# Kernel optimization log

Hardware: AMD Instinct MI355X
Metric: run time of the kernel (lower is better)

The kernel has to match this reference:

```python
import jax, jax.numpy as jnp
import numpy as np

EMBED_DIM = 768
NUM_HEADS = 12
HEAD_DIM = EMBED_DIM // NUM_HEADS


def setup_inputs() -> dict:
    key = jax.random.key(0)
    ks = jax.random.split(key, 6)
    B, N = 8, 1024
    x = jax.random.normal(ks[0], (B, N, EMBED_DIM), dtype=jnp.float32)
    pos_embedding = jax.random.normal(ks[1], (1, NUM_HEADS, N, N), dtype=jnp.float32)
    s_in = 1.0 / np.sqrt(EMBED_DIM)
    W_qkv = jax.random.normal(ks[2], (EMBED_DIM, 3 * EMBED_DIM), dtype=jnp.float32) * s_in
    b_qkv = jnp.zeros((3 * EMBED_DIM,), dtype=jnp.float32)
    W_proj = jax.random.normal(ks[3], (EMBED_DIM, EMBED_DIM), dtype=jnp.float32) * s_in
    b_proj = jnp.zeros((EMBED_DIM,), dtype=jnp.float32)
    return {"x": x, "pos_embedding": pos_embedding, "W_qkv": W_qkv,
            "b_qkv": b_qkv, "W_proj": W_proj, "b_proj": b_proj}


def reference(x, pos_embedding, W_qkv, b_qkv, W_proj, b_proj):
    B, N, C = x.shape
    H, D = NUM_HEADS, HEAD_DIM
    qkv = x @ W_qkv + b_qkv                      # [B,N,3C]
    qkv = qkv.reshape(B, N, 3, H, D)
    q = qkv[:, :, 0].transpose(0, 2, 1, 3)       # [B,H,N,D]
    k = qkv[:, :, 1].transpose(0, 2, 1, 3)
    v = qkv[:, :, 2].transpose(0, 2, 1, 3)
    # NOTE: bias is added BEFORE scaling, matching the original module.
    scores = (jnp.einsum('bhnd,bhmd->bhnm', q, k) + pos_embedding) / jnp.sqrt(
        jnp.asarray(D, dtype=x.dtype))
    attn = jax.nn.softmax(scores, axis=-1)       # dropout is identity in eval
    out = jnp.einsum('bhnm,bhmd->bhnd', attn, v)
    out = out.transpose(0, 2, 1, 3).reshape(B, N, C)
    return out @ W_proj + b_proj
```

## Files before the change

kernel.cpp:

```cpp
#include <hip/hip_runtime.h>

#define SEQ   1024
#define HEADS 12
#define CDIM  768
#define BATCH 8

#define QSCALE 0.18033688011112042f

typedef __attribute__((ext_vector_type(8))) short bf16x8;
typedef __attribute__((ext_vector_type(4))) float f32x4;
typedef __attribute__((ext_vector_type(16))) float f32x16;
typedef __attribute__((ext_vector_type(4))) float float4v;
typedef __attribute__((ext_vector_type(4))) short short4v;

__device__ __forceinline__ void gload_lds16(const void* g, void* l) {
  __builtin_amdgcn_global_load_lds(
      (const __attribute__((address_space(1))) unsigned int*)g,
      (__attribute__((address_space(3))) unsigned int*)l, 16, 0, 0);
}

__device__ __forceinline__ unsigned short f2bf(float f) {
  union { float f; unsigned u; } v; v.f = f;
  unsigned r = v.u + 0x7fff + ((v.u >> 16) & 1);
  return (unsigned short)(r >> 16);
}

__device__ __forceinline__ unsigned cvtpk(float a, float b) {
  unsigned r;
  asm("v_cvt_pk_bf16_f32 %0, %1, %2" : "=v"(r) : "v"(a), "v"(b));
  return r;
}

__device__ __forceinline__ float bfsel(unsigned u, int odd) {
  union { unsigned u; float f; } v;
  v.u = odd ? (u & 0xffff0000u) : (u << 16);
  return v.f;
}

__global__ __launch_bounds__(256) void prep_x_kernel(const float* __restrict__ x,
                                                     short* __restrict__ A) {
  int i = blockIdx.x * 256 + threadIdx.x;
  int r = i / 192;
  int c4 = (i % 192) * 4;
  float4v xv = *(const float4v*)(x + (size_t)r * 768 + c4);
  short4v hi;
#pragma unroll
  for (int j = 0; j < 4; ++j) hi[j] = (short)f2bf(xv[j]);
  *(short4v*)(A + (size_t)r * 768 + c4) = hi;
}

__global__ __launch_bounds__(256) void prep_w_kernel(const float* __restrict__ W,
                                                     short* __restrict__ Bt) {
  __shared__ float tile[64][65];
  int k0 = blockIdx.x * 64;
  int n0 = blockIdx.y * 64;
  int t = threadIdx.x;
#pragma unroll
  for (int it = 0; it < 16; ++it) {
    int r = it * 4 + (t >> 6);
    int c = t & 63;
    tile[r][c] = W[(size_t)(k0 + r) * 2304 + n0 + c];
  }
  __syncthreads();
#pragma unroll
  for (int it = 0; it < 16; ++it) {
    int nr = it * 4 + (t >> 6);
    int kc = t & 63;
    Bt[(size_t)(n0 + nr) * 768 + k0 + kc] = (short)f2bf(tile[kc][nr]);
  }
}

__global__ __launch_bounds__(256) void prep_wp_kernel(const float* __restrict__ W,
                                                      short* __restrict__ Bt) {
  __shared__ float tile[64][65];
  int k0 = blockIdx.x * 64;
  int n0 = blockIdx.y * 64;
  int t = threadIdx.x;
#pragma unroll
  for (int it = 0; it < 16; ++it) {
    int r = it * 4 + (t >> 6);
    int c = t & 63;
    tile[r][c] = W[(size_t)(k0 + r) * 768 + n0 + c];
  }
  __syncthreads();
#pragma unroll
  for (int it = 0; it < 16; ++it) {
    int nr = it * 4 + (t >> 6);
    int kc = t & 63;
    Bt[(size_t)(n0 + nr) * 768 + k0 + kc] = (short)f2bf(tile[kc][nr]);
  }
}

__global__ __launch_bounds__(256) void prep_pos_kernel(const float* __restrict__ P,
                                                       short* __restrict__ PB) {
  int t = blockIdx.x * 256 + threadIdx.x;
  int lane = t & 63;
  int jh   = (t >> 6) & 1;
  int i0   = (t >> 7) & 1;
  int w    = (t >> 8) & 3;
  int ti   = (t >> 10) & 15;
  int qblk = (t >> 14) & 7;
  int h    = t >> 17;
  int c5 = lane & 31, g1 = lane >> 5;
  int q = qblk * 128 + w * 32 + c5;
  const float* src = P + ((size_t)h * SEQ + q) * SEQ
                     + ti * 64 + i0 * 32 + 4 * g1 + 16 * jh;
  float4v v0 = *(const float4v*)(src);
  float4v v1 = *(const float4v*)(src + 8);
  union { short s[8]; bf16x8 v; } o;
#pragma unroll
  for (int p = 0; p < 4; ++p) {
    o.s[p]     = (short)f2bf(v0[p] * QSCALE);
    o.s[4 + p] = (short)f2bf(v1[p] * QSCALE);
  }
  *(bf16x8*)(PB + (size_t)t * 8) = o.v;
}

template <int MODE>
__global__ __launch_bounds__(512, 6) void gemm_kernel(
    const short* __restrict__ A, const short* __restrict__ Bt,
    const float* __restrict__ bias,
    short* __restrict__ outQ, short* __restrict__ outK, short* __restrict__ outVT,
    float* __restrict__ outF) {
  constexpr int NBLK = (MODE == 1) ? 18 : 6;
  constexpr int CHUNK = (MODE == 1) ? 144 : 48;
  const int bid = blockIdx.x;
  const int lb = (bid & 7) * CHUNK + (bid >> 3);
  const int n0 = (lb % NBLK) * 128;
  const int m0 = (lb / NBLK) * 128;

  __shared__ short lds[3 * 8192];

  const int tid = threadIdx.x;
  const int lane = tid & 63;
  const int w = tid >> 6;
  const int wr = (w & 1) * 64;
  const int wc = (w >> 1) * 32;
  const int c = lane & 15, g = lane >> 4;
  f32x4 acc[4][2];
#pragma unroll
  for (int mi = 0; mi < 4; ++mi)
#pragma unroll
    for (int ni = 0; ni < 2; ++ni) acc[mi][ni] = (f32x4){0.f, 0.f, 0.f, 0.f};

  auto STAGE = [&](int buf, int k0) {
    short* base = lds + buf * 8192;
    int row = tid >> 2;
    int us = (tid & 3) ^ (row & 3);
    gload_lds16(A + (size_t)(m0 + row) * 768 + k0 + us * 8, base + w * 512);
    gload_lds16(Bt + (size_t)(n0 + row) * 768 + k0 + us * 8, base + 4096 + w * 512);
  };

  STAGE(0, 0);
  STAGE(1, 32);
  asm volatile("s_waitcnt vmcnt(2)" ::: "memory");
  __builtin_amdgcn_sched_barrier(0);
  __builtin_amdgcn_s_barrier();

  for (int t = 0; t < 24; ++t) {
    if (t < 22) STAGE((t + 2) % 3, (t + 2) * 32);
    const char* Ab = (const char*)(lds + (t % 3) * 8192);
    const char* Bb = Ab + 8192;
    __builtin_amdgcn_s_setprio(1);
    bf16x8 af[4], bfv[2];
#pragma unroll
    for (int mi = 0; mi < 4; ++mi) {
      int row = wr + mi * 16 + c;
      af[mi] = *(const bf16x8*)(Ab + row * 64 + ((g ^ (row & 3)) * 16));
    }
#pragma unroll
    for (int ni = 0; ni < 2; ++ni) {
      int row = wc + ni * 16 + c;
      bfv[ni] = *(const bf16x8*)(Bb + row * 64 + ((g ^ (row & 3)) * 16));
    }
#pragma unroll
    for (int mi = 0; mi < 4; ++mi)
#pragma unroll
      for (int ni = 0; ni < 2; ++ni)
        acc[mi][ni] = __builtin_amdgcn_mfma_f32_16x16x32_bf16(
            af[mi], bfv[ni], acc[mi][ni], 0, 0, 0);
    __builtin_amdgcn_s_setprio(0);
    if (t < 23) {
      if (t < 22) asm volatile("s_waitcnt vmcnt(2)" ::: "memory");
      else        asm volatile("s_waitcnt vmcnt(0)" ::: "memory");
      __builtin_amdgcn_sched_barrier(0);
      __builtin_amdgcn_s_barrier();
    }
  }

  if (MODE == 1) {
    const int three = n0 / 768;
    const int nb = n0 - three * 768;
#pragma unroll
    for (int mi = 0; mi < 4; ++mi)
#pragma unroll
      for (int ni = 0; ni < 2; ++ni)
#pragma unroll
        for (int j = 0; j < 4; ++j) {
          int row = m0 + wr + mi * 16 + (g << 2) + j;
          int col = n0 + wc + ni * 16 + c;
          float v = acc[mi][ni][j] + bias[col];
          int rem = nb + wc + ni * 16 + c;
          int hh = rem >> 6, d = rem & 63;
          int b = row >> 10, n = row & 1023;
          size_t bh = (size_t)(b * 12 + hh);
          if (three == 0)      outQ[(bh * 1024 + n) * 64 + d] = (short)f2bf(v * QSCALE);
          else if (three == 1) outK[(bh * 1024 + n) * 64 + d] = (short)f2bf(v);
          else                 outVT[(bh * 64 + d) * 1024 + n] = (short)f2bf(v);
        }
  } else {
#pragma unroll
    for (int mi = 0; mi < 4; ++mi)
#pragma unroll
      for (int ni = 0; ni < 2; ++ni)
#pragma unroll
        for (int j = 0; j < 4; ++j) {
          int row = m0 + wr + mi * 16 + (g << 2) + j;
          int col = n0 + wc + ni * 16 + c;
          outF[(size_t)row * 768 + col] = acc[mi][ni][j] + bias[col];
        }
  }
}

#define MKFRAG(B, pA, pB, pC, pD)                                    \
  { unsigned x0 = (pA), y0 = (pC), x1 = (pB), y1 = (pD);             \
    asm("v_permlane32_swap_b32 %0, %1" : "+v"(x0), "+v"(y0));        \
    asm("v_permlane32_swap_b32 %0, %1" : "+v"(x1), "+v"(y1));        \
    B.u[0] = x0; B.u[1] = x1; B.u[2] = y0; B.u[3] = y1; }

__global__ __launch_bounds__(256, 3) void attn_kernel(
    const short* __restrict__ qb, const short* __restrict__ kb,
    const short* __restrict__ vtb, const short* __restrict__ posb,
    short* __restrict__ outb) {
  const int bid = blockIdx.x;
  const int lb = (bid & 7) * 96 + (bid >> 3);
  const int qblk = lb & 7;
  const int hb = lb >> 3;
  const int h = hb >> 3, b = hb & 7;

  const int tid = threadIdx.x, lane = tid & 63, w = tid >> 6;
  const int c5 = lane & 31, g1 = lane >> 5;
  const size_t bh = (size_t)(b * 12 + h);
  const short* Q = qb + bh * SEQ * 64;
  const short* K = kb + bh * SEQ * 64;
  const short* VT = vtb + bh * 64 * SEQ;
  const int q0w = qblk * 128 + w * 32;

  const short* pwb = posb + (size_t)h * 1048576 + (size_t)qblk * 131072
                     + w * 2048 + lane * 8;

  __shared__ short kls[3 * 4096];
  __shared__ short vls[3 * 4096];

  bf16x8 qf[4];
#pragma unroll
  for (int kd = 0; kd < 4; ++kd)
    qf[kd] = *(const bf16x8*)(Q + (size_t)(q0w + c5) * 64 + kd * 16 + g1 * 8);

  f32x16 o0, o1;
#pragma unroll
  for (int i = 0; i < 16; ++i) { o0[i] = 0.f; o1[i] = 0.f; }
  float lsum = 0.f;

  auto STAGE = [&](short* kb_, short* vb_, int kv0) {
    int r0 = w * 8 + (lane >> 3);
    int u0 = (lane & 7) ^ (r0 & 7);
    gload_lds16(K + (size_t)(kv0 + r0) * 64 + u0 * 8, kb_ + w * 512);
    gload_lds16(K + (size_t)(kv0 + 32 + r0) * 64 + u0 * 8, kb_ + 2048 + w * 512);
    gload_lds16(VT + (size_t)r0 * SEQ + kv0 + u0 * 8, vb_ + w * 512);
    gload_lds16(VT + (size_t)(32 + r0) * SEQ + kv0 + u0 * 8, vb_ + 2048 + w * 512);
  };

  short* kbuf0 = kls;        short* vbuf0 = vls;
  short* kbuf1 = kls + 4096; short* vbuf1 = vls + 4096;
  short* kbuf2 = kls + 8192; short* vbuf2 = vls + 8192;

  STAGE(kbuf0, vbuf0, 0);
  STAGE(kbuf1, vbuf1, 64);
  asm volatile("s_waitcnt vmcnt(4)" ::: "memory");
  __builtin_amdgcn_sched_barrier(0);
  __builtin_amdgcn_s_barrier();

  for (int ti = 0; ti < 16; ++ti) {
    const int kv0 = ti * 64;

    union { bf16x8 v; unsigned u[4]; } ua0, ua1, ub0, ub1;
    ua0.v = *(const bf16x8*)(pwb + ti * 8192);
    ua1.v = *(const bf16x8*)(pwb + ti * 8192 + 512);
    ub0.v = *(const bf16x8*)(pwb + ti * 8192 + 1024);
    ub1.v = *(const bf16x8*)(pwb + ti * 8192 + 1536);
    asm volatile("" ::: "memory");
    if (ti < 14) STAGE(kbuf2, vbuf2, kv0 + 128);

    const short* kc = kbuf0;
    const short* vc = vbuf0;

    f32x16 p0, p1;
#pragma unroll
    for (int i = 0; i < 16; ++i) { p0[i] = 0.f; p1[i] = 0.f; }
    __builtin_amdgcn_s_setprio(1);
#pragma unroll
    for (int kd = 0; kd < 4; ++kd) {
      int off0 = (c5 * 128 + kd * 32 + g1 * 16) ^ ((c5 & 7) << 4);
      int off1 = ((32 + c5) * 128 + kd * 32 + g1 * 16) ^ ((c5 & 7) << 4);
      bf16x8 kf0 = *(const bf16x8*)((const char*)kc + off0);
      bf16x8 kf1 = *(const bf16x8*)((const char*)kc + off1);
      p0 = __builtin_amdgcn_mfma_f32_32x32x16_bf16(kf0, qf[kd], p0, 0, 0, 0);
      p1 = __builtin_amdgcn_mfma_f32_32x32x16_bf16(kf1, qf[kd], p1, 0, 0, 0);
    }
    __builtin_amdgcn_s_setprio(0);

#pragma unroll
    for (int r = 0; r < 16; ++r) {
      unsigned wa = (r < 8) ? ua0.u[(r >> 1) & 3] : ua1.u[(r >> 1) & 3];
      unsigned wb = (r < 8) ? ub0.u[(r >> 1) & 3] : ub1.u[(r >> 1) & 3];
      float a = exp2f(p0[r] + bfsel(wa, r & 1));
      float bq = exp2f(p1[r] + bfsel(wb, r & 1));
      p0[r] = a; p1[r] = bq;
      lsum += a + bq;
    }

    unsigned pk0[8], pk1[8];
#pragma unroll
    for (int m = 0; m < 4; ++m) {
      pk0[2 * m]     = cvtpk(p0[4 * m],     p0[4 * m + 1]);
      pk0[2 * m + 1] = cvtpk(p0[4 * m + 2], p0[4 * m + 3]);
      pk1[2 * m]     = cvtpk(p1[4 * m],     p1[4 * m + 1]);
      pk1[2 * m + 1] = cvtpk(p1[4 * m + 2], p1[4 * m + 3]);
    }

    union bb { bf16x8 v; unsigned u[4]; } B0, B1, B2, B3;
    MKFRAG(B0, pk0[0], pk0[1], pk0[2], pk0[3]);
    MKFRAG(B1, pk0[4], pk0[5], pk0[6], pk0[7]);
    MKFRAG(B2, pk1[0], pk1[1], pk1[2], pk1[3]);
    MKFRAG(B3, pk1[4], pk1[5], pk1[6], pk1[7]);

    __builtin_amdgcn_s_setprio(1);
#define PVSTEP(Bv, s)                                                        \
    { int o0f = (c5 * 128 + (s) * 32 + g1 * 16) ^ ((c5 & 7) << 4);           \
      int o1f = ((32 + c5) * 128 + (s) * 32 + g1 * 16) ^ ((c5 & 7) << 4);    \
      bf16x8 vf0 = *(const bf16x8*)((const char*)vc + o0f);                  \
      bf16x8 vf1 = *(const bf16x8*)((const char*)vc + o1f);                  \
      o0 = __builtin_amdgcn_mfma_f32_32x32x16_bf16(vf0, Bv.v, o0, 0, 0, 0);  \
      o1 = __builtin_amdgcn_mfma_f32_32x32x16_bf16(vf1, Bv.v, o1, 0, 0, 0); }
    PVSTEP(B0, 0); PVSTEP(B1, 1); PVSTEP(B2, 2); PVSTEP(B3, 3);
#undef PVSTEP
    __builtin_amdgcn_s_setprio(0);

    short* tk = kbuf0; kbuf0 = kbuf1; kbuf1 = kbuf2; kbuf2 = tk;
    short* tv = vbuf0; vbuf0 = vbuf1; vbuf1 = vbuf2; vbuf2 = tv;

    if (ti < 15) {
      if (ti < 14) asm volatile("s_waitcnt vmcnt(4)" ::: "memory");
      else         asm volatile("s_waitcnt vmcnt(0)" ::: "memory");
      __builtin_amdgcn_sched_barrier(0);
      __builtin_amdgcn_s_barrier();
    }
  }

  lsum += __shfl_xor(lsum, 32);
  float inv = 1.0f / lsum;
  size_t obase = (size_t)(b * SEQ + q0w + c5) * 768 + h * 64 + g1 * 4;
#pragma unroll
  for (int m = 0; m < 4; ++m) {
    short4v ov0, ov1;
#pragma unroll
    for (int j = 0; j < 4; ++j) {
      ov0[j] = (short)f2bf(o0[4 * m + j] * inv);
      ov1[j] = (short)f2bf(o1[4 * m + j] * inv);
    }
    *(short4v*)(outb + obase + m * 8) = ov0;
    *(short4v*)(outb + obase + 32 + m * 8) = ov1;
  }
}

extern "C" void kernel_launch(void* const* d_in, const int* in_sizes, int n_in,
                              void* d_out, int out_size, void* d_ws, size_t ws_size,
                              hipStream_t stream) {
  const float* x      = (const float*)d_in[0];
  const float* pos    = (const float*)d_in[1];
  const float* W_qkv  = (const float*)d_in[2];
  const float* b_qkv  = (const float*)d_in[3];
  const float* W_proj = (const float*)d_in[4];
  const float* b_proj = (const float*)d_in[5];
  float* out = (float*)d_out;

  char* ws = (char*)d_ws;
  short* A       = (short*)(ws);
  short* attnbuf = (short*)(ws);
  short* Bt      = (short*)(ws + 12582912);
  short* wpt     = (short*)(ws + 16121856);
  short* qbuf    = (short*)(ws + 17301504);
  short* kbuf    = (short*)(ws + 29884416);
  short* vtbuf   = (short*)(ws + 42467328);
  short* posb    = (short*)(ws + 55050240);

  prep_x_kernel<<<6144, 256, 0, stream>>>(x, A);
  prep_w_kernel<<<dim3(12, 36), 256, 0, stream>>>(W_qkv, Bt);
  prep_wp_kernel<<<dim3(12, 12), 256, 0, stream>>>(W_proj, wpt);
  prep_pos_kernel<<<6144, 256, 0, stream>>>(pos, posb);
  gemm_kernel<1><<<1152, 512, 0, stream>>>(A, Bt, b_qkv,
                                           qbuf, kbuf, vtbuf, nullptr);
  attn_kernel<<<768, 256, 0, stream>>>(qbuf, kbuf, vtbuf, posb, attnbuf);
  gemm_kernel<2><<<384, 512, 0, stream>>>(attnbuf, wpt, b_proj,
                                          nullptr, nullptr, nullptr, out);
}
```

Baseline: 153.6 us.

## Use 256x256 tiles with double-buffered LDS for the QKV projection GEMM

Splits the templated GEMM into a dedicated QKV kernel that computes 256x256 output tiles per 512-thread block, with a larger LDS double buffer (128KB) and swizzled fragment loads. Loads for the next k-tile are interleaved across four sub-phases of MFMA work. The aim is more operand reuse per global byte and fewer blocks. The cost is lower occupancy (2 blocks/CU bound, 288 blocks on a large-CU GPU, so a possible tail or underfill) and higher register pressure from 32 accumulators per lane.

```diff
diff --git a/kernel.cpp b/kernel.cpp
--- a/kernel.cpp
+++ b/kernel.cpp
@@ -116,14 +116,132 @@
   *(bf16x8*)(PB + (size_t)t * 8) = o.v;
 }
 
-template <int MODE>
-__global__ __launch_bounds__(512, 6) void gemm_kernel(
+__global__ __launch_bounds__(512, 2) void gemm1_kernel(
     const short* __restrict__ A, const short* __restrict__ Bt,
     const float* __restrict__ bias,
-    short* __restrict__ outQ, short* __restrict__ outK, short* __restrict__ outVT,
-    float* __restrict__ outF) {
-  constexpr int NBLK = (MODE == 1) ? 18 : 6;
-  constexpr int CHUNK = (MODE == 1) ? 144 : 48;
+    short* __restrict__ outQ, short* __restrict__ outK, short* __restrict__ outVT) {
+  const int bid = blockIdx.x;
+  const int lb = (bid & 7) * 36 + (bid >> 3);
+  const int nt = lb % 9, mt = lb / 9;
+  const int n0 = nt * 256, m0 = mt * 256;
+
+  __shared__ short lds[65536];
+
+  const int tid = threadIdx.x;
+  const int lane = tid & 63;
+  const int w = tid >> 6;
+  const int wm = w >> 2;
+  const int wn = w & 3;
+  const int c = lane & 15, g = lane >> 4;
+
+  f32x4 acc[8][4];
+#pragma unroll
+  for (int i = 0; i < 8; ++i)
+#pragma unroll
+    for (int v = 0; v < 4; ++v) acc[i][v] = (f32x4){0.f, 0.f, 0.f, 0.f};
+
+  const int rl = lane >> 3;
+  const int su = (lane & 7) ^ rl;
+
+  auto STAGE_A = [&](int db, int h, int kt) {
+    short* dst = lds + db * 32768 + h * 8192;
+    const short* src = A + (size_t)(m0 + h * 128) * 768 + kt * 64 + su * 8;
+    gload_lds16(src + (size_t)((w * 2 + 0) * 8 + rl) * 768, dst + (w * 2 + 0) * 512);
+    gload_lds16(src + (size_t)((w * 2 + 1) * 8 + rl) * 768, dst + (w * 2 + 1) * 512);
+  };
+  auto STAGE_B = [&](int db, int h, int kt) {
+    short* dst = lds + db * 32768 + 16384 + h * 8192;
+    const short* src = Bt + (size_t)(n0 + h * 128) * 768 + kt * 64 + su * 8;
+    gload_lds16(src + (size_t)((w * 2 + 0) * 8 + rl) * 768, dst + (w * 2 + 0) * 512);
+    gload_lds16(src + (size_t)((w * 2 + 1) * 8 + rl) * 768, dst + (w * 2 + 1) * 512);
+  };
+
+  STAGE_A(0, 0, 0); STAGE_A(0, 1, 0); STAGE_B(0, 0, 0); STAGE_B(0, 1, 0);
+  asm volatile("s_waitcnt vmcnt(2)" ::: "memory");
+  __builtin_amdgcn_sched_barrier(0);
+  __builtin_amdgcn_s_barrier();
+
+  for (int kt = 0; kt < 12; ++kt) {
+    const int d = kt & 1;
+    const char* Ab = (const char*)(lds + d * 32768 + wm * 8192);
+    const char* Bb = (const char*)(lds + d * 32768 + 16384);
+    bf16x8 af[4][2];
+#pragma unroll
+    for (int p = 0; p < 4; ++p) {
+      const int al = p >> 1, be = p & 1;
+      if (kt < 11) {
+        if (p == 0)      STAGE_A(d ^ 1, 0, kt + 1);
+        else if (p == 1) STAGE_A(d ^ 1, 1, kt + 1);
+        else if (p == 2) STAGE_B(d ^ 1, 0, kt + 1);
+        else             STAGE_B(d ^ 1, 1, kt + 1);
+      }
+      if (be == 0) {
+#pragma unroll
+        for (int i = 0; i < 4; ++i) {
+          int rloc = (al * 4 + i) * 16 + c;
+          int sw = (rloc & 7) << 4;
+#pragma unroll
+          for (int kk = 0; kk < 2; ++kk)
+            af[i][kk] = *(const bf16x8*)(Ab + ((rloc * 128 + kk * 64 + g * 16) ^ sw));
+        }
+      }
+      bf16x8 bfv[2][2];
+#pragma unroll
+      for (int v = 0; v < 2; ++v) {
+        int rloc = v * 64 + wn * 16 + c;
+        int sw = (rloc & 7) << 4;
+#pragma unroll
+        for (int kk = 0; kk < 2; ++kk)
+          bfv[v][kk] = *(const bf16x8*)(Bb + be * 16384 +
+                                        ((rloc * 128 + kk * 64 + g * 16) ^ sw));
+      }
+      __builtin_amdgcn_s_setprio(1);
+#pragma unroll
+      for (int i = 0; i < 4; ++i)
+#pragma unroll
+        for (int v = 0; v < 2; ++v)
+#pragma unroll
+          for (int kk = 0; kk < 2; ++kk)
+            acc[al * 4 + i][be * 2 + v] = __builtin_amdgcn_mfma_f32_16x16x32_bf16(
+                af[i][kk], bfv[v][kk], acc[al * 4 + i][be * 2 + v], 0, 0, 0);
+      __builtin_amdgcn_s_setprio(0);
+      if (p == 0) {
+        if (kt < 11) asm volatile("s_waitcnt vmcnt(2)" ::: "memory");
+        else         asm volatile("s_waitcnt vmcnt(0)" ::: "memory");
+      } else if (p == 3 && kt < 11) {
+        asm volatile("s_waitcnt vmcnt(2)" ::: "memory");
+      }
+      __builtin_amdgcn_sched_barrier(0);
+      __builtin_amdgcn_s_barrier();
+    }
+  }
+
+  const int three = (n0 >= 1536) ? 2 : ((n0 >= 768) ? 1 : 0);
+  const int nb = n0 - three * 768;
+#pragma unroll
+  for (int mi = 0; mi < 8; ++mi)
+#pragma unroll
+    for (int nu = 0; nu < 4; ++nu)
+#pragma unroll
+      for (int j = 0; j < 4; ++j) {
+        int row = m0 + wm * 128 + mi * 16 + (g << 2) + j;
+        int col = n0 + nu * 64 + wn * 16 + c;
+        float v = acc[mi][nu][j] + bias[col];
+        int rem = nb + nu * 64 + wn * 16 + c;
+        int hh = rem >> 6, dd = rem & 63;
+        int b = row >> 10, n = row & 1023;
+        size_t bh = (size_t)(b * 12 + hh);
+        if (three == 0)      outQ[(bh * 1024 + n) * 64 + dd] = (short)f2bf(v * QSCALE);
+        else if (three == 1) outK[(bh * 1024 + n) * 64 + dd] = (short)f2bf(v);
+        else                 outVT[(bh * 64 + dd) * 1024 + n] = (short)f2bf(v);
+      }
+}
+
+__global__ __launch_bounds__(512, 6) void gemm2_kernel(
+    const short* __restrict__ A, const short* __restrict__ Bt,
+    const float* __restrict__ bias, float* __restrict__ outF) {
+  constexpr int NBLK = 6;
+  constexpr int CHUNK = 48;
   const int bid = blockIdx.x;
   const int lb = (bid & 7) * CHUNK + (bid >> 3);
   const int n0 = (lb % NBLK) * 128;
@@ -188,38 +306,16 @@
     }
   }
 
-  if (MODE == 1) {
-    const int three = n0 / 768;
-    const int nb = n0 - three * 768;
-#pragma unroll
-    for (int mi = 0; mi < 4; ++mi)
-#pragma unroll
-      for (int ni = 0; ni < 2; ++ni)
-#pragma unroll
-        for (int j = 0; j < 4; ++j) {
-          int row = m0 + wr + mi * 16 + (g << 2) + j;
-          int col = n0 + wc + ni * 16 + c;
-          float v = acc[mi][ni][j] + bias[col];
-          int rem = nb + wc + ni * 16 + c;
-          int hh = rem >> 6, d = rem & 63;
-          int b = row >> 10, n = row & 1023;
-          size_t bh = (size_t)(b * 12 + hh);
-          if (three == 0)      outQ[(bh * 1024 + n) * 64 + d] = (short)f2bf(v * QSCALE);
-          else if (three == 1) outK[(bh * 1024 + n) * 64 + d] = (short)f2bf(v);
-          else                 outVT[(bh * 64 + d) * 1024 + n] = (short)f2bf(v);
-        }
-  } else {
-#pragma unroll
-    for (int mi = 0; mi < 4; ++mi)
-#pragma unroll
-      for (int ni = 0; ni < 2; ++ni)
-#pragma unroll
-        for (int j = 0; j < 4; ++j) {
-          int row = m0 + wr + mi * 16 + (g << 2) + j;
-          int col = n0 + wc + ni * 16 + c;
-          outF[(size_t)row * 768 + col] = acc[mi][ni][j] + bias[col];
-        }
-  }
+#pragma unroll
+  for (int mi = 0; mi < 4; ++mi)
+#pragma unroll
+    for (int ni = 0; ni < 2; ++ni)
+#pragma unroll
+      for (int j = 0; j < 4; ++j) {
+        int row = m0 + wr + mi * 16 + (g << 2) + j;
+        int col = n0 + wc + ni * 16 + c;
+        outF[(size_t)row * 768 + col] = acc[mi][ni][j] + bias[col];
+      }
 }
 
 #define MKFRAG(B, pA, pB, pC, pD)                                    \
@@ -399,9 +495,7 @@
   prep_w_kernel<<<dim3(12, 36), 256, 0, stream>>>(W_qkv, Bt);
   prep_wp_kernel<<<dim3(12, 12), 256, 0, stream>>>(W_proj, wpt);
   prep_pos_kernel<<<6144, 256, 0, stream>>>(pos, posb);
-  gemm_kernel<1><<<1152, 512, 0, stream>>>(A, Bt, b_qkv,
-                                           qbuf, kbuf, vtbuf, nullptr);
+  gemm1_kernel<<<288, 512, 0, stream>>>(A, Bt, b_qkv, qbuf, kbuf, vtbuf);
   attn_kernel<<<768, 256, 0, stream>>>(qbuf, kbuf, vtbuf, posb, attnbuf);
-  gemm_kernel<2><<<384, 512, 0, stream>>>(attnbuf, wpt, b_proj,
-                                          nullptr, nullptr, nullptr, out);
-}
+  gemm2_kernel<<<384, 512, 0, stream>>>(attnbuf, wpt, b_proj, out);
+}
```

Measured after the change: 172.9 us. +12.6%, slower.
